# Kernel tuning notes

Measured on AMD Instinct MI355X. Metric: run time of the kernel, lower is better.

Reference implementation:

```python
import jax, jax.numpy as jnp
import numpy as np
import math

B, N, D = 128, 64, 2
H, M, L = 64, 64, 2
OMEGA = 1.0


def setup_inputs() -> dict:
    key = jax.random.key(0)
    ks = jax.random.split(key, 32)
    s = 0.1  # param scale
    rn = lambda k, shp: jax.random.normal(k, shp, dtype=jnp.float32) * s
    inp = {
        "x": jax.random.normal(ks[0], (B, N, D), dtype=jnp.float32),
        "spin": jnp.zeros((B, N, 1), jnp.float32),
        "node_w1": rn(ks[1], (D + 1, H)), "node_b1": rn(ks[2], (H,)),
        "node_w2": rn(ks[3], (H, H)), "node_b2": rn(ks[4], (H,)),
        "edge_w1": rn(ks[5], (D + 2, M)), "edge_b1": rn(ks[6], (M,)),
        "edge_w2": rn(ks[7], (M, M)), "edge_b2": rn(ks[8], (M,)),
        "v2e_w1": rn(ks[9], (L, H + M, M)), "v2e_b1": rn(ks[10], (L, M)),
        "v2e_w2": rn(ks[11], (L, M, M)), "v2e_b2": rn(ks[12], (L, M)),
        "e2v_w1": rn(ks[13], (L, M, H)), "e2v_b1": rn(ks[14], (L, H)),
        "e2v_w2": rn(ks[15], (L, H, H)), "e2v_b2": rn(ks[16], (L, H)),
        "head_w1": rn(ks[17], (H, H)), "head_b1": rn(ks[18], (H,)),
        "head_w2": rn(ks[19], (H, D)), "head_b2": rn(ks[20], (D,)),
        # bf_scale_init=0.3 -> softplus-inverse
        "scale": jnp.array([math.log(math.exp(0.3) - 1.0)], jnp.float32),
    }
    return inp


def _mlp(x, w1, b1, w2, b2, act):
    return act(x @ w1 + b1) @ w2 + b2


def reference(x, spin, node_w1, node_b1, node_w2, node_b2,
              edge_w1, edge_b1, edge_w2, edge_b2,
              v2e_w1, v2e_b1, v2e_w2, v2e_b2,
              e2v_w1, e2v_b1, e2v_w2, e2v_b2,
              head_w1, head_b1, head_w2, head_b2, scale):
    gelu = lambda t: jax.nn.gelu(t, approximate=False)  # torch exact GELU
    b, n, d = x.shape
    xs = x * jnp.float32(math.sqrt(OMEGA))
    # node embedding: [B,N,H]
    hv = _mlp(jnp.concatenate([xs, spin], -1), node_w1, node_b1, node_w2, node_b2, gelu)
    # dense pairwise edge features; dr[b,i,j] = xs[b,j] - xs[b,i]
    dr = xs[:, None, :, :] - xs[:, :, None, :]            # [B,N,N,D]
    r2 = jnp.sum(dr * dr, axis=-1, keepdims=True)          # [B,N,N,1]
    rr = jnp.sqrt(r2 + 1e-12)
    he = _mlp(jnp.concatenate([dr, rr, r2], -1), edge_w1, edge_b1, edge_w2, edge_b2, gelu)  # [B,N,N,M]
    # mask excludes self-edges (i==j) from aggregation (they were never created
    # in the original edge list; their dense entries never influence off-diag values)
    mask = (1.0 - jnp.eye(n, dtype=x.dtype))[None, :, :, None]
    inv = jnp.float32(1.0 / max(n - 1, 1))
    for l in range(v2e_w1.shape[0]):
        hvb = jnp.broadcast_to(hv[:, :, None, :], (b, n, n, hv.shape[-1]))  # source node i
        he = _mlp(jnp.concatenate([hvb, he], -1), v2e_w1[l], v2e_b1[l], v2e_w2[l], v2e_b2[l], gelu)
        m = _mlp(he, e2v_w1[l], e2v_b1[l], e2v_w2[l], e2v_b2[l], gelu)      # [B,N,N,H]
        hv = hv + jnp.sum(m * mask, axis=1) * inv           # scatter-add over sources i into j
    dx = _mlp(hv, head_w1, head_b1, head_w2, head_b2, jnp.tanh) * jax.nn.softplus(scale[0])
    return dx - jnp.mean(dx, axis=1, keepdims=True)
```

## Files before the change

kernel.cpp:

```cpp
#include <hip/hip_runtime.h>
#include <math.h>


typedef unsigned short u16;
typedef unsigned int u32;
typedef _Float16 half8 __attribute__((ext_vector_type(8)));
typedef __attribute__((ext_vector_type(4))) float floatx4;

#define TS 72

__device__ __forceinline__ float2 gelu2(float2 x) {
    const float K = 0.70710678118654752f;
    float ux = x.x * K,        uy = x.y * K;
    float sx = fabsf(ux),      sy = fabsf(uy);
    float tx = __builtin_amdgcn_rcpf(fmaf(0.3275911f, sx, 1.0f));
    float ty = __builtin_amdgcn_rcpf(fmaf(0.3275911f, sy, 1.0f));
    float Px = tx * fmaf(tx, fmaf(tx, fmaf(tx, fmaf(tx, 1.061405429f, -1.453152027f),
                                           1.421413741f), -0.284496736f), 0.254829592f);
    float Py = ty * fmaf(ty, fmaf(ty, fmaf(ty, fmaf(ty, 1.061405429f, -1.453152027f),
                                           1.421413741f), -0.284496736f), 0.254829592f);
    float ex = __expf(-sx * sx);
    float ey = __expf(-sy * sy);
    float rx = copysignf(fmaf(-Px, ex, 1.0f), ux);
    float ry = copysignf(fmaf(-Py, ey, 1.0f), uy);
    return make_float2(0.5f * x.x * (1.0f + rx), 0.5f * x.y * (1.0f + ry));
}
__device__ __forceinline__ float gelu_f(float x) {
    float u = x * 0.70710678118654752f;
    float s = fabsf(u);
    float t = __builtin_amdgcn_rcpf(fmaf(0.3275911f, s, 1.0f));
    float P = t * fmaf(t, fmaf(t, fmaf(t, fmaf(t, 1.061405429f, -1.453152027f),
                                        1.421413741f), -0.284496736f), 0.254829592f);
    float r = copysignf(fmaf(-P, __expf(-s * s), 1.0f), u);
    return 0.5f * x * (1.0f + r);
}

__global__ __launch_bounds__(256) void k_pre(
    const float* w0, const float* w1, const float* w2, const float* w3,
    const float* w4, const float* w5, const float* w6,
    const float* u2_0, const float* u2_1, const float* w1n, const float* hw1,
    _Float16* __restrict__ WF,
    float* __restrict__ u2_0T, float* __restrict__ u2_1T,
    float* __restrict__ w1nT, float* __restrict__ hw1T,
    const float* __restrict__ x, const float* __restrict__ spin,
    const float* __restrict__ nw1, const float* __restrict__ nb1,
    const float* __restrict__ nw2, const float* __restrict__ nb2,
    const float* __restrict__ w1_0, const float* __restrict__ b1_0,
    float* __restrict__ hv, float* __restrict__ p0)
{
    int blk = blockIdx.x;
    if (blk < 112) {
        int idx = blk * 256 + threadIdx.x;
        int s = idx >> 12, r = idx & 4095, k = r >> 6, n = r & 63;
        const float* W = s==0?w0: s==1?w1: s==2?w2: s==3?w3: s==4?w4: s==5?w5: w6;
        int kc = k >> 5, q = (k >> 3) & 3, jj = k & 7;
        WF[(((s * 2 + kc) * 64 + n) * 4 + q) * 8 + jj] = (_Float16)W[k * 64 + n];
    } else if (blk < 176) {
        int idx = (blk - 112) * 256 + threadIdx.x;
        int s = idx >> 12, r = idx & 4095, m = r >> 6, tc = r & 63;
        const float* W = s==0?u2_0: s==1?u2_1: s==2?w1n: hw1;
        float* WT      = s==0?u2_0T: s==1?u2_1T: s==2?w1nT: hw1T;
        WT[tc * 64 + m] = W[m * 64 + tc];
    } else {
        __shared__ float a[4][64];
        __shared__ float shv[4][64];
        int w = threadIdx.x >> 6, h = threadIdx.x & 63;
        int node = (blk - 176) * 4 + w;
        float2 xv = ((const float2*)x)[node];
        float sp = spin[node];
        float z = fmaf(xv.x, nw1[h], fmaf(xv.y, nw1[64 + h], fmaf(sp, nw1[128 + h], nb1[h])));
        a[w][h] = gelu_f(z);
        float acc = nb2[h];
        for (int k = 0; k < 64; ++k) acc = fmaf(a[w][k], nw2[k * 64 + h], acc);
        hv[node * 64 + h] = acc;
        shv[w][h] = acc;
        float pa = b1_0[h];
        for (int k = 0; k < 64; ++k) pa = fmaf(shv[w][k], w1_0[k * 64 + h], pa);
        p0[node * 64 + h] = pa;
    }
}

__device__ __forceinline__ void mfma_acc(
    const _Float16* __restrict__ tA, const _Float16* __restrict__ WF,
    int stage, int c, int quad, int nn, floatx4 acc[4])
{
    int sA = ((nn >> 2) & 3) << 3;
    #pragma unroll
    for (int kc = 0; kc < 2; ++kc) {
        half8 bf = *(const half8*)(WF + (((stage * 2 + kc) * 64 + c) * 4 + quad) * 8);
        int k0 = (kc * 32 + quad * 8) ^ sA;
        #pragma unroll
        for (int mt = 0; mt < 4; ++mt) {
            half8 af = *(const half8*)(tA + (mt * 16 + nn) * TS + k0);
            acc[mt] = __builtin_amdgcn_mfma_f32_16x16x32_f16(af, bf, acc[mt], 0, 0, 0);
        }
    }
}

__device__ __forceinline__ void init_bias(floatx4 acc[4], float bc) {
    #pragma unroll
    for (int mt = 0; mt < 4; ++mt) acc[mt] = (floatx4){bc, bc, bc, bc};
}
__device__ __forceinline__ void init_p(floatx4 acc[4], const float* __restrict__ p,
                                       int rowbase, int c, int quad) {
    #pragma unroll
    for (int mt = 0; mt < 4; ++mt)
        #pragma unroll
        for (int r = 0; r < 4; ++r)
            acc[mt][r] = p[(rowbase + mt * 16 + quad * 4 + r) * 64 + c];
}

__global__ __launch_bounds__(256, 8) void k_L0(
    const float* __restrict__ x,
    const float* __restrict__ ew1, const float* __restrict__ eb1,
    const float* __restrict__ eb2,
    const float* __restrict__ p0, const float* __restrict__ b2_0,
    const float* __restrict__ c1_0,
    const float* __restrict__ u2_0T, const float* __restrict__ c2_0,
    const _Float16* __restrict__ WF,
    const float* __restrict__ hv0, float* __restrict__ hv1,
    const float* __restrict__ w1nT, const float* __restrict__ b1n,
    float* __restrict__ p1,
    u16* __restrict__ he0g)
{
    __shared__ __align__(16) _Float16 tA[64 * TS];
    __shared__ float sgeo[256];
    __shared__ float sS[64];
    __shared__ float shv[64];
    int t = threadIdx.x, w = t >> 6, L = t & 63;
    int nn = L & 15, quad = L >> 4;
    int c = w * 16 + nn;
    int cw = c ^ (quad << 3);
    int b = blockIdx.x >> 6, j = blockIdx.x & 63;

    if (t < 64) {
        float2 xi = ((const float2*)x)[b * 64 + t];
        float2 xj = ((const float2*)x)[b * 64 + j];
        float d0 = xj.x - xi.x, d1 = xj.y - xi.y;
        float r2 = fmaf(d0, d0, d1 * d1);
        sgeo[t] = d0; sgeo[64 + t] = d1; sgeo[128 + t] = sqrtf(r2 + 1e-12f); sgeo[192 + t] = r2;
    }
    __syncthreads();
    {
        int m = t & 63, i0 = t >> 6;
        float wa = ew1[m], wb = ew1[64 + m], wc = ew1[128 + m], wd = ew1[192 + m], bm = eb1[m];
        #pragma unroll
        for (int k = 0; k < 16; k += 2) {
            int ia = i0 + k * 4, ib = i0 + (k + 1) * 4;
            float za = fmaf(sgeo[ia], wa, fmaf(sgeo[64 + ia], wb,
                       fmaf(sgeo[128 + ia], wc, fmaf(sgeo[192 + ia], wd, bm))));
            float zb = fmaf(sgeo[ib], wa, fmaf(sgeo[64 + ib], wb,
                       fmaf(sgeo[128 + ib], wc, fmaf(sgeo[192 + ib], wd, bm))));
            float2 g = gelu2(make_float2(za, zb));
            tA[ia * TS + (m ^ (((ia >> 2) & 3) << 3))] = (_Float16)g.x;
            tA[ib * TS + (m ^ (((ib >> 2) & 3) << 3))] = (_Float16)g.y;
        }
    }
    __syncthreads();

    floatx4 acc[4];
    init_bias(acc, eb2[c]);
    mfma_acc(tA, WF, 0, c, quad, nn, acc);
    __syncthreads();
    #pragma unroll
    for (int mt = 0; mt < 4; ++mt)
        #pragma unroll
        for (int r = 0; r < 4; ++r)
            tA[(mt * 16 + quad * 4 + r) * TS + cw] = (_Float16)acc[mt][r];
    __syncthreads();
    init_p(acc, p0, b * 64, c, quad);
    mfma_acc(tA, WF, 1, c, quad, nn, acc);
    __syncthreads();
    #pragma unroll
    for (int mt = 0; mt < 4; ++mt)
        #pragma unroll
        for (int rp = 0; rp < 4; rp += 2) {
            float2 g = gelu2(make_float2(acc[mt][rp], acc[mt][rp + 1]));
            tA[(mt * 16 + quad * 4 + rp) * TS + cw]     = (_Float16)g.x;
            tA[(mt * 16 + quad * 4 + rp + 1) * TS + cw] = (_Float16)g.y;
        }
    __syncthreads();
    init_bias(acc, b2_0[c]);
    mfma_acc(tA, WF, 2, c, quad, nn, acc);
    __syncthreads();
    {
        u16* dst = he0g + (size_t)blockIdx.x * 4096;
        #pragma unroll
        for (int mt = 0; mt < 4; ++mt)
            #pragma unroll
            for (int r = 0; r < 4; ++r) {
                int i = mt * 16 + quad * 4 + r;
                _Float16 hvv = (_Float16)acc[mt][r];
                tA[i * TS + cw] = hvv;
                dst[i * 64 + cw] = __builtin_bit_cast(u16, hvv);
            }
    }
    __syncthreads();
    init_bias(acc, c1_0[c]);
    mfma_acc(tA, WF, 3, c, quad, nn, acc);
    {
        float s = 0.f;
        #pragma unroll
        for (int mt = 0; mt < 4; ++mt)
            #pragma unroll
            for (int rp = 0; rp < 4; rp += 2) {
                int i = mt * 16 + quad * 4 + rp;
                float2 g = gelu2(make_float2(acc[mt][rp], acc[mt][rp + 1]));
                s += (i == j ? 0.f : g.x) + (i + 1 == j ? 0.f : g.y);
            }
        s += __shfl_xor(s, 16);
        s += __shfl_xor(s, 32);
        if (quad == 0) sS[c] = s;
    }
    __syncthreads();
    if (t < 64) {
        const float4* sv4 = (const float4*)sS;
        const float4* uv4 = (const float4*)(u2_0T + t * 64);
        float g = 0.f;
        #pragma unroll
        for (int m4 = 0; m4 < 16; ++m4) {
            float4 sv = sv4[m4], uv = uv4[m4];
            g = fmaf(sv.x, uv.x, fmaf(sv.y, uv.y, fmaf(sv.z, uv.z, fmaf(sv.w, uv.w, g))));
        }
        int o = blockIdx.x * 64 + t;
        float hvv = hv0[o] + g * (1.0f / 63.0f) + c2_0[t];
        hv1[o] = hvv;
        shv[t] = hvv;
        const float4* hv4 = (const float4*)shv;
        const float4* wv4 = (const float4*)(w1nT + t * 64);
        float pa = b1n[t];
        #pragma unroll
        for (int m4 = 0; m4 < 16; ++m4) {
            float4 sv = hv4[m4], uv = wv4[m4];
            pa = fmaf(sv.x, uv.x, fmaf(sv.y, uv.y, fmaf(sv.z, uv.z, fmaf(sv.w, uv.w, pa))));
        }
        p1[o] = pa;
    }
}

__global__ __launch_bounds__(256, 8) void k_L1(
    const u16* __restrict__ he0g,
    const float* __restrict__ p1, const float* __restrict__ b2_1,
    const float* __restrict__ c1_1,
    const float* __restrict__ u2_1T, const float* __restrict__ c2_1,
    const _Float16* __restrict__ WF,
    const float* __restrict__ hv1,
    const float* __restrict__ hw1T, const float* __restrict__ hb1,
    const float* __restrict__ hw2, const float* __restrict__ hb2,
    const float* __restrict__ scale, float* __restrict__ dx)
{
    __shared__ __align__(16) _Float16 tA[64 * TS];
    __shared__ float sS[64];
    __shared__ float shv[64];
    int t = threadIdx.x, w = t >> 6, L = t & 63;
    int nn = L & 15, quad = L >> 4;
    int c = w * 16 + nn;
    int cw = c ^ (quad << 3);
    int b = blockIdx.x >> 6, j = blockIdx.x & 63;

    {
        const u32* src = (const u32*)(he0g + (size_t)blockIdx.x * 4096);
        for (int qq = t; qq < 2048; qq += 256) {
            u32 v = src[qq];
            int i = qq >> 5, m2 = (qq & 31) * 2;
            *(u32*)((u16*)tA + i * TS + m2) = v;
        }
    }
    __syncthreads();

    floatx4 acc[4];
    init_p(acc, p1, b * 64, c, quad);
    mfma_acc(tA, WF, 4, c, quad, nn, acc);
    __syncthreads();
    #pragma unroll
    for (int mt = 0; mt < 4; ++mt)
        #pragma unroll
        for (int rp = 0; rp < 4; rp += 2) {
            float2 g = gelu2(make_float2(acc[mt][rp], acc[mt][rp + 1]));
            tA[(mt * 16 + quad * 4 + rp) * TS + cw]     = (_Float16)g.x;
            tA[(mt * 16 + quad * 4 + rp + 1) * TS + cw] = (_Float16)g.y;
        }
    __syncthreads();
    init_bias(acc, b2_1[c]);
    mfma_acc(tA, WF, 5, c, quad, nn, acc);
    __syncthreads();
    #pragma unroll
    for (int mt = 0; mt < 4; ++mt)
        #pragma unroll
        for (int r = 0; r < 4; ++r)
            tA[(mt * 16 + quad * 4 + r) * TS + cw] = (_Float16)acc[mt][r];
    __syncthreads();
    init_bias(acc, c1_1[c]);
    mfma_acc(tA, WF, 6, c, quad, nn, acc);
    {
        float s = 0.f;
        #pragma unroll
        for (int mt = 0; mt < 4; ++mt)
            #pragma unroll
            for (int rp = 0; rp < 4; rp += 2) {
                int i = mt * 16 + quad * 4 + rp;
                float2 g = gelu2(make_float2(acc[mt][rp], acc[mt][rp + 1]));
                s += (i == j ? 0.f : g.x) + (i + 1 == j ? 0.f : g.y);
            }
        s += __shfl_xor(s, 16);
        s += __shfl_xor(s, 32);
        if (quad == 0) sS[c] = s;
    }
    __syncthreads();
    if (t < 64) {
        const float4* sv4 = (const float4*)sS;
        const float4* uv4 = (const float4*)(u2_1T + t * 64);
        float g = 0.f;
        #pragma unroll
        for (int m4 = 0; m4 < 16; ++m4) {
            float4 sv = sv4[m4], uv = uv4[m4];
            g = fmaf(sv.x, uv.x, fmaf(sv.y, uv.y, fmaf(sv.z, uv.z, fmaf(sv.w, uv.w, g))));
        }
        float hv2 = hv1[blockIdx.x * 64 + t] + g * (1.0f / 63.0f) + c2_1[t];
        shv[t] = hv2;
        const float4* hv4 = (const float4*)shv;
        const float4* wv4 = (const float4*)(hw1T + t * 64);
        float a = hb1[t];
        #pragma unroll
        for (int m4 = 0; m4 < 16; ++m4) {
            float4 sv = hv4[m4], uv = wv4[m4];
            a = fmaf(sv.x, uv.x, fmaf(sv.y, uv.y, fmaf(sv.z, uv.z, fmaf(sv.w, uv.w, a))));
        }
        float t1 = tanhf(a);
        float d0 = t1 * hw2[t * 2], d1 = t1 * hw2[t * 2 + 1];
        #pragma unroll
        for (int off = 1; off <= 32; off <<= 1) { d0 += __shfl_xor(d0, off); d1 += __shfl_xor(d1, off); }
        if (t == 0) {
            float sp = log1pf(__expf(scale[0]));
            dx[blockIdx.x * 2 + 0] = (d0 + hb2[0]) * sp;
            dx[blockIdx.x * 2 + 1] = (d1 + hb2[1]) * sp;
        }
    }
}

__global__ __launch_bounds__(64) void k_mean(
    const float* __restrict__ dx, float* __restrict__ out)
{
    __shared__ float s0[64], s1[64];
    int b = blockIdx.x, j = threadIdx.x;
    float2 d = ((const float2*)dx)[b * 64 + j];
    s0[j] = d.x; s1[j] = d.y;
    __syncthreads();
    float m0 = 0.f, m1 = 0.f;
    for (int q = 0; q < 64; ++q) { m0 += s0[q]; m1 += s1[q]; }
    ((float2*)out)[b * 64 + j] = make_float2(d.x - m0 * (1.0f / 64.0f), d.y - m1 * (1.0f / 64.0f));
}

__global__ void k_beacon(float* out, float code) { out[0] = code; }

extern "C" void kernel_launch(void* const* d_in, const int* in_sizes, int n_in,
                              void* d_out, int out_size, void* d_ws, size_t ws_size,
                              hipStream_t stream)
{
    static const int exp_sizes[23] = {
        16384, 8192, 192, 64, 4096, 64,
        256, 64, 4096, 64,
        16384, 128, 8192, 128,
        8192, 128, 8192, 128,
        4096, 64, 128, 2, 1
    };
    float* hv0 = (float*)d_ws;
    float* hv1 = hv0 + 524288;
    float* p0  = hv1 + 524288;
    float* p1  = p0  + 524288;
    float* dx  = p1  + 524288;
    float* u2_0T = dx + 16384;
    float* u2_1T = u2_0T + 4096;
    float* w1nT  = u2_1T + 4096;
    float* hw1T  = w1nT + 4096;
    _Float16* WF = (_Float16*)(hw1T + 4096);
    u16* he0g  = (u16*)(WF + 28672);
    const size_t need = (size_t)((char*)(he0g + 33554432) - (char*)d_ws);

    int bad = -1;
    if (n_in != 23 || out_size != 16384) bad = 98;
    else if (ws_size < need) bad = 97;
    else for (int i = 0; i < 23; ++i)
        if (in_sizes[i] != exp_sizes[i]) { bad = i; break; }
    if (bad >= 0) {
        k_beacon<<<1, 1, 0, stream>>>((float*)d_out, 2e6f + bad * 1e4f);
        return;
    }

    const float* x      = (const float*)d_in[0];
    const float* spin   = (const float*)d_in[1];
    const float* nw1    = (const float*)d_in[2];
    const float* nb1    = (const float*)d_in[3];
    const float* nw2    = (const float*)d_in[4];
    const float* nb2    = (const float*)d_in[5];
    const float* ew1    = (const float*)d_in[6];
    const float* eb1    = (const float*)d_in[7];
    const float* ew2    = (const float*)d_in[8];
    const float* eb2    = (const float*)d_in[9];
    const float* v2e_w1 = (const float*)d_in[10];
    const float* v2e_b1 = (const float*)d_in[11];
    const float* v2e_w2 = (const float*)d_in[12];
    const float* v2e_b2 = (const float*)d_in[13];
    const float* e2v_w1 = (const float*)d_in[14];
    const float* e2v_b1 = (const float*)d_in[15];
    const float* e2v_w2 = (const float*)d_in[16];
    const float* e2v_b2 = (const float*)d_in[17];
    const float* hw1    = (const float*)d_in[18];
    const float* hb1    = (const float*)d_in[19];
    const float* hw2    = (const float*)d_in[20];
    const float* hb2    = (const float*)d_in[21];
    const float* scale  = (const float*)d_in[22];

    k_pre<<<2224, 256, 0, stream>>>(
        ew2, v2e_w1 + 4096, v2e_w2, e2v_w1, v2e_w1 + 12288, v2e_w2 + 4096, e2v_w1 + 4096,
        e2v_w2, e2v_w2 + 4096, v2e_w1 + 8192, hw1,
        WF, u2_0T, u2_1T, w1nT, hw1T,
        x, spin, nw1, nb1, nw2, nb2, v2e_w1, v2e_b1, hv0, p0);
    k_L0<<<8192, 256, 0, stream>>>(x, ew1, eb1, eb2,
        p0, v2e_b2, e2v_b1, u2_0T, e2v_b2,
        WF, hv0, hv1,
        w1nT, v2e_b1 + 64, p1,
        he0g);
    k_L1<<<8192, 256, 0, stream>>>(he0g,
        p1, v2e_b2 + 64, e2v_b1 + 64, u2_1T, e2v_b2 + 64,
        WF, hv1, hw1T, hb1, hw2, hb2, scale, dx);
    k_mean<<<128, 64, 0, stream>>>(dx, (float*)d_out);
}
```

Baseline: 256.0 us.

## Fold consecutive linear layers into precomputed fused weights and biases

Back-to-back linear maps with no activation between them (edge w2 into v2e w1, v2e w2 into e2v w1) are multiplied together in a prep kernel. The per-edge kernels then run 2 MFMA GEMM stages per layer instead of 3–4, and drop the matching LDS round-trips and barriers. The prep is split into two kernels because the node embedding now needs a folded bias. Folding weights changes fp16 rounding of the intermediates, and the exact gelu2 pair helper is replaced by a scalar gelu.

```diff
diff --git a/kernel.cpp b/kernel.cpp
--- a/kernel.cpp
+++ b/kernel.cpp
@@ -9,22 +9,6 @@
 
 #define TS 72
 
-__device__ __forceinline__ float2 gelu2(float2 x) {
-    const float K = 0.70710678118654752f;
-    float ux = x.x * K,        uy = x.y * K;
-    float sx = fabsf(ux),      sy = fabsf(uy);
-    float tx = __builtin_amdgcn_rcpf(fmaf(0.3275911f, sx, 1.0f));
-    float ty = __builtin_amdgcn_rcpf(fmaf(0.3275911f, sy, 1.0f));
-    float Px = tx * fmaf(tx, fmaf(tx, fmaf(tx, fmaf(tx, 1.061405429f, -1.453152027f),
-                                           1.421413741f), -0.284496736f), 0.254829592f);
-    float Py = ty * fmaf(ty, fmaf(ty, fmaf(ty, fmaf(ty, 1.061405429f, -1.453152027f),
-                                           1.421413741f), -0.284496736f), 0.254829592f);
-    float ex = __expf(-sx * sx);
-    float ey = __expf(-sy * sy);
-    float rx = copysignf(fmaf(-Px, ex, 1.0f), ux);
-    float ry = copysignf(fmaf(-Py, ey, 1.0f), uy);
-    return make_float2(0.5f * x.x * (1.0f + rx), 0.5f * x.y * (1.0f + ry));
-}
 __device__ __forceinline__ float gelu_f(float x) {
     float u = x * 0.70710678118654752f;
     float s = fabsf(u);
@@ -35,49 +19,78 @@
     return 0.5f * x * (1.0f + r);
 }
 
-__global__ __launch_bounds__(256) void k_pre(
-    const float* w0, const float* w1, const float* w2, const float* w3,
-    const float* w4, const float* w5, const float* w6,
-    const float* u2_0, const float* u2_1, const float* w1n, const float* hw1,
+__global__ __launch_bounds__(256) void k_pre1(
+    const float* __restrict__ ew2, const float* __restrict__ w1he0,
+    const float* __restrict__ w2_0, const float* __restrict__ u1_0,
+    const float* __restrict__ w1he1, const float* __restrict__ w2_1,
+    const float* __restrict__ u1_1,
+    const float* __restrict__ eb2, const float* __restrict__ b2_0,
+    const float* __restrict__ c1_0, const float* __restrict__ b2_1,
+    const float* __restrict__ c1_1,
+    const float* __restrict__ u2_0, const float* __restrict__ u2_1,
+    const float* __restrict__ w1n, const float* __restrict__ hw1,
     _Float16* __restrict__ WF,
+    float* __restrict__ biasA, float* __restrict__ biasB,
+    float* __restrict__ biasC, float* __restrict__ biasD,
     float* __restrict__ u2_0T, float* __restrict__ u2_1T,
-    float* __restrict__ w1nT, float* __restrict__ hw1T,
+    float* __restrict__ w1nT, float* __restrict__ hw1T)
+{
+    int blk = blockIdx.x;
+    if (blk < 64) {
+        int s = blk >> 4;
+        int idx = (blk & 15) * 256 + threadIdx.x;
+        int k = idx >> 6, n = idx & 63;
+        const float *A, *Bm;
+        if (s == 0)      { A = ew2;  Bm = w1he0; }
+        else if (s == 1) { A = w2_0; Bm = u1_0;  }
+        else if (s == 2) { A = w2_0; Bm = w1he1; }
+        else             { A = w2_1; Bm = u1_1;  }
+        float acc = 0.f;
+        for (int q = 0; q < 64; ++q) acc = fmaf(A[k * 64 + q], Bm[q * 64 + n], acc);
+        int kc = k >> 5, qd = (k >> 3) & 3, jj = k & 7;
+        WF[(((s * 2 + kc) * 64 + n) * 4 + qd) * 8 + jj] = (_Float16)acc;
+    } else if (blk == 64) {
+        int s = threadIdx.x >> 6, cc = threadIdx.x & 63;
+        const float *bv, *Bm, *add; float* dst;
+        if (s == 0)      { bv = eb2;  Bm = w1he0; add = nullptr; dst = biasA; }
+        else if (s == 1) { bv = b2_0; Bm = u1_0;  add = c1_0;    dst = biasB; }
+        else if (s == 2) { bv = b2_0; Bm = w1he1; add = nullptr; dst = biasC; }
+        else             { bv = b2_1; Bm = u1_1;  add = c1_1;    dst = biasD; }
+        float acc = add ? add[cc] : 0.f;
+        for (int q = 0; q < 64; ++q) acc = fmaf(bv[q], Bm[q * 64 + cc], acc);
+        dst[cc] = acc;
+    } else {
+        int idx = (blk - 65) * 256 + threadIdx.x;
+        int s = idx >> 12, r = idx & 4095, m = r >> 6, tc = r & 63;
+        const float* W = s == 0 ? u2_0 : s == 1 ? u2_1 : s == 2 ? w1n : hw1;
+        float* WT      = s == 0 ? u2_0T : s == 1 ? u2_1T : s == 2 ? w1nT : hw1T;
+        WT[tc * 64 + m] = W[m * 64 + tc];
+    }
+}
+
+__global__ __launch_bounds__(256) void k_pre2(
     const float* __restrict__ x, const float* __restrict__ spin,
     const float* __restrict__ nw1, const float* __restrict__ nb1,
     const float* __restrict__ nw2, const float* __restrict__ nb2,
     const float* __restrict__ w1_0, const float* __restrict__ b1_0,
+    const float* __restrict__ biasA,
     float* __restrict__ hv, float* __restrict__ p0)
 {
-    int blk = blockIdx.x;
-    if (blk < 112) {
-        int idx = blk * 256 + threadIdx.x;
-        int s = idx >> 12, r = idx & 4095, k = r >> 6, n = r & 63;
-        const float* W = s==0?w0: s==1?w1: s==2?w2: s==3?w3: s==4?w4: s==5?w5: w6;
-        int kc = k >> 5, q = (k >> 3) & 3, jj = k & 7;
-        WF[(((s * 2 + kc) * 64 + n) * 4 + q) * 8 + jj] = (_Float16)W[k * 64 + n];
-    } else if (blk < 176) {
-        int idx = (blk - 112) * 256 + threadIdx.x;
-        int s = idx >> 12, r = idx & 4095, m = r >> 6, tc = r & 63;
-        const float* W = s==0?u2_0: s==1?u2_1: s==2?w1n: hw1;
-        float* WT      = s==0?u2_0T: s==1?u2_1T: s==2?w1nT: hw1T;
-        WT[tc * 64 + m] = W[m * 64 + tc];
-    } else {
-        __shared__ float a[4][64];
-        __shared__ float shv[4][64];
-        int w = threadIdx.x >> 6, h = threadIdx.x & 63;
-        int node = (blk - 176) * 4 + w;
-        float2 xv = ((const float2*)x)[node];
-        float sp = spin[node];
-        float z = fmaf(xv.x, nw1[h], fmaf(xv.y, nw1[64 + h], fmaf(sp, nw1[128 + h], nb1[h])));
-        a[w][h] = gelu_f(z);
-        float acc = nb2[h];
-        for (int k = 0; k < 64; ++k) acc = fmaf(a[w][k], nw2[k * 64 + h], acc);
-        hv[node * 64 + h] = acc;
-        shv[w][h] = acc;
-        float pa = b1_0[h];
-        for (int k = 0; k < 64; ++k) pa = fmaf(shv[w][k], w1_0[k * 64 + h], pa);
-        p0[node * 64 + h] = pa;
-    }
+    __shared__ float a[4][64];
+    __shared__ float shv[4][64];
+    int w = threadIdx.x >> 6, h = threadIdx.x & 63;
+    int node = blockIdx.x * 4 + w;
+    float2 xv = ((const float2*)x)[node];
+    float sp = spin[node];
+    float z = fmaf(xv.x, nw1[h], fmaf(xv.y, nw1[64 + h], fmaf(sp, nw1[128 + h], nb1[h])));
+    a[w][h] = gelu_f(z);
+    float acc = nb2[h];
+    for (int k = 0; k < 64; ++k) acc = fmaf(a[w][k], nw2[k * 64 + h], acc);
+    hv[node * 64 + h] = acc;
+    shv[w][h] = acc;
+    float pa = b1_0[h] + biasA[h];
+    for (int k = 0; k < 64; ++k) pa = fmaf(shv[w][k], w1_0[k * 64 + h], pa);
+    p0[node * 64 + h] = pa;
 }
 
 __device__ __forceinline__ void mfma_acc(
@@ -113,13 +126,13 @@
 __global__ __launch_bounds__(256, 8) void k_L0(
     const float* __restrict__ x,
     const float* __restrict__ ew1, const float* __restrict__ eb1,
-    const float* __restrict__ eb2,
-    const float* __restrict__ p0, const float* __restrict__ b2_0,
-    const float* __restrict__ c1_0,
+    const float* __restrict__ p0,
+    const float* __restrict__ biasB,
     const float* __restrict__ u2_0T, const float* __restrict__ c2_0,
     const _Float16* __restrict__ WF,
     const float* __restrict__ hv0, float* __restrict__ hv1,
     const float* __restrict__ w1nT, const float* __restrict__ b1n,
+    const float* __restrict__ biasC,
     float* __restrict__ p1,
     u16* __restrict__ he0g)
 {
@@ -145,43 +158,18 @@
         int m = t & 63, i0 = t >> 6;
         float wa = ew1[m], wb = ew1[64 + m], wc = ew1[128 + m], wd = ew1[192 + m], bm = eb1[m];
         #pragma unroll
-        for (int k = 0; k < 16; k += 2) {
-            int ia = i0 + k * 4, ib = i0 + (k + 1) * 4;
-            float za = fmaf(sgeo[ia], wa, fmaf(sgeo[64 + ia], wb,
-                       fmaf(sgeo[128 + ia], wc, fmaf(sgeo[192 + ia], wd, bm))));
-            float zb = fmaf(sgeo[ib], wa, fmaf(sgeo[64 + ib], wb,
-                       fmaf(sgeo[128 + ib], wc, fmaf(sgeo[192 + ib], wd, bm))));
-            float2 g = gelu2(make_float2(za, zb));
-            tA[ia * TS + (m ^ (((ia >> 2) & 3) << 3))] = (_Float16)g.x;
-            tA[ib * TS + (m ^ (((ib >> 2) & 3) << 3))] = (_Float16)g.y;
+        for (int k = 0; k < 16; ++k) {
+            int i = i0 + k * 4;
+            float z = fmaf(sgeo[i], wa, fmaf(sgeo[64 + i], wb,
+                      fmaf(sgeo[128 + i], wc, fmaf(sgeo[192 + i], wd, bm))));
+            tA[i * TS + (m ^ (((i >> 2) & 3) << 3))] = (_Float16)gelu_f(z);
         }
     }
     __syncthreads();
 
     floatx4 acc[4];
-    init_bias(acc, eb2[c]);
+    init_p(acc, p0, b * 64, c, quad);
     mfma_acc(tA, WF, 0, c, quad, nn, acc);
-    __syncthreads();
-    #pragma unroll
-    for (int mt = 0; mt < 4; ++mt)
-        #pragma unroll
-        for (int r = 0; r < 4; ++r)
-            tA[(mt * 16 + quad * 4 + r) * TS + cw] = (_Float16)acc[mt][r];
-    __syncthreads();
-    init_p(acc, p0, b * 64, c, quad);
-    mfma_acc(tA, WF, 1, c, quad, nn, acc);
-    __syncthreads();
-    #pragma unroll
-    for (int mt = 0; mt < 4; ++mt)
-        #pragma unroll
-        for (int rp = 0; rp < 4; rp += 2) {
-            float2 g = gelu2(make_float2(acc[mt][rp], acc[mt][rp + 1]));
-            tA[(mt * 16 + quad * 4 + rp) * TS + cw]     = (_Float16)g.x;
-            tA[(mt * 16 + quad * 4 + rp + 1) * TS + cw] = (_Float16)g.y;
-        }
-    __syncthreads();
-    init_bias(acc, b2_0[c]);
-    mfma_acc(tA, WF, 2, c, quad, nn, acc);
     __syncthreads();
     {
         u16* dst = he0g + (size_t)blockIdx.x * 4096;
@@ -190,23 +178,23 @@
             #pragma unroll
             for (int r = 0; r < 4; ++r) {
                 int i = mt * 16 + quad * 4 + r;
-                _Float16 hvv = (_Float16)acc[mt][r];
-                tA[i * TS + cw] = hvv;
-                dst[i * 64 + cw] = __builtin_bit_cast(u16, hvv);
+                _Float16 y = (_Float16)gelu_f(acc[mt][r]);
+                tA[i * TS + cw] = y;
+                dst[i * 64 + cw] = __builtin_bit_cast(u16, y);
             }
     }
     __syncthreads();
-    init_bias(acc, c1_0[c]);
-    mfma_acc(tA, WF, 3, c, quad, nn, acc);
+    init_bias(acc, biasB[c]);
+    mfma_acc(tA, WF, 1, c, quad, nn, acc);
     {
         float s = 0.f;
         #pragma unroll
         for (int mt = 0; mt < 4; ++mt)
             #pragma unroll
-            for (int rp = 0; rp < 4; rp += 2) {
-                int i = mt * 16 + quad * 4 + rp;
-                float2 g = gelu2(make_float2(acc[mt][rp], acc[mt][rp + 1]));
-                s += (i == j ? 0.f : g.x) + (i + 1 == j ? 0.f : g.y);
+            for (int r = 0; r < 4; ++r) {
+                int i = mt * 16 + quad * 4 + r;
+                float g = gelu_f(acc[mt][r]);
+                s += (i == j) ? 0.f : g;
             }
         s += __shfl_xor(s, 16);
         s += __shfl_xor(s, 32);
@@ -228,7 +216,7 @@
         shv[t] = hvv;
         const float4* hv4 = (const float4*)shv;
         const float4* wv4 = (const float4*)(w1nT + t * 64);
-        float pa = b1n[t];
+        float pa = b1n[t] + biasC[t];
         #pragma unroll
         for (int m4 = 0; m4 < 16; ++m4) {
             float4 sv = hv4[m4], uv = wv4[m4];
@@ -240,8 +228,8 @@
 
 __global__ __launch_bounds__(256, 8) void k_L1(
     const u16* __restrict__ he0g,
-    const float* __restrict__ p1, const float* __restrict__ b2_1,
-    const float* __restrict__ c1_1,
+    const float* __restrict__ p1,
+    const float* __restrict__ biasD,
     const float* __restrict__ u2_1T, const float* __restrict__ c2_1,
     const _Float16* __restrict__ WF,
     const float* __restrict__ hv1,
@@ -270,37 +258,25 @@
 
     floatx4 acc[4];
     init_p(acc, p1, b * 64, c, quad);
-    mfma_acc(tA, WF, 4, c, quad, nn, acc);
+    mfma_acc(tA, WF, 2, c, quad, nn, acc);
     __syncthreads();
     #pragma unroll
     for (int mt = 0; mt < 4; ++mt)
         #pragma unroll
-        for (int rp = 0; rp < 4; rp += 2) {
-            float2 g = gelu2(make_float2(acc[mt][rp], acc[mt][rp + 1]));
-            tA[(mt * 16 + quad * 4 + rp) * TS + cw]     = (_Float16)g.x;
-            tA[(mt * 16 + quad * 4 + rp + 1) * TS + cw] = (_Float16)g.y;
-        }
-    __syncthreads();
-    init_bias(acc, b2_1[c]);
-    mfma_acc(tA, WF, 5, c, quad, nn, acc);
-    __syncthreads();
-    #pragma unroll
-    for (int mt = 0; mt < 4; ++mt)
-        #pragma unroll
         for (int r = 0; r < 4; ++r)
-            tA[(mt * 16 + quad * 4 + r) * TS + cw] = (_Float16)acc[mt][r];
-    __syncthreads();
-    init_bias(acc, c1_1[c]);
-    mfma_acc(tA, WF, 6, c, quad, nn, acc);
+            tA[(mt * 16 + quad * 4 + r) * TS + cw] = (_Float16)gelu_f(acc[mt][r]);
+    __syncthreads();
+    init_bias(acc, biasD[c]);
+    mfma_acc(tA, WF, 3, c, quad, nn, acc);
     {
         float s = 0.f;
         #pragma unroll
         for (int mt = 0; mt < 4; ++mt)
             #pragma unroll
-            for (int rp = 0; rp < 4; rp += 2) {
-                int i = mt * 16 + quad * 4 + rp;
-                float2 g = gelu2(make_float2(acc[mt][rp], acc[mt][rp + 1]));
-                s += (i == j ? 0.f : g.x) + (i + 1 == j ? 0.f : g.y);
+            for (int r = 0; r < 4; ++r) {
+                int i = mt * 16 + quad * 4 + r;
+                float g = gelu_f(acc[mt][r]);
+                s += (i == j) ? 0.f : g;
             }
         s += __shfl_xor(s, 16);
         s += __shfl_xor(s, 32);
@@ -373,8 +349,12 @@
     float* u2_1T = u2_0T + 4096;
     float* w1nT  = u2_1T + 4096;
     float* hw1T  = w1nT + 4096;
-    _Float16* WF = (_Float16*)(hw1T + 4096);
-    u16* he0g  = (u16*)(WF + 28672);
+    float* biasA = hw1T + 4096;
+    float* biasB = biasA + 64;
+    float* biasC = biasB + 64;
+    float* biasD = biasC + 64;
+    _Float16* WF = (_Float16*)(biasD + 64);
+    u16* he0g  = (u16*)(WF + 16384);
     const size_t need = (size_t)((char*)(he0g + 33554432) - (char*)d_ws);
 
     int bad = -1;
@@ -411,18 +391,22 @@
     const float* hb2    = (const float*)d_in[21];
     const float* scale  = (const float*)d_in[22];
 
-    k_pre<<<2224, 256, 0, stream>>>(
-        ew2, v2e_w1 + 4096, v2e_w2, e2v_w1, v2e_w1 + 12288, v2e_w2 + 4096, e2v_w1 + 4096,
+    k_pre1<<<129, 256, 0, stream>>>(
+        ew2, v2e_w1 + 4096, v2e_w2, e2v_w1,
+        v2e_w1 + 12288, v2e_w2 + 4096, e2v_w1 + 4096,
+        eb2, v2e_b2, e2v_b1, v2e_b2 + 64, e2v_b1 + 64,
         e2v_w2, e2v_w2 + 4096, v2e_w1 + 8192, hw1,
-        WF, u2_0T, u2_1T, w1nT, hw1T,
-        x, spin, nw1, nb1, nw2, nb2, v2e_w1, v2e_b1, hv0, p0);
-    k_L0<<<8192, 256, 0, stream>>>(x, ew1, eb1, eb2,
-        p0, v2e_b2, e2v_b1, u2_0T, e2v_b2,
+        WF, biasA, biasB, biasC, biasD,
+        u2_0T, u2_1T, w1nT, hw1T);
+    k_pre2<<<2048, 256, 0, stream>>>(x, spin, nw1, nb1, nw2, nb2,
+                                     v2e_w1, v2e_b1, biasA, hv0, p0);
+    k_L0<<<8192, 256, 0, stream>>>(x, ew1, eb1,
+        p0, biasB, u2_0T, e2v_b2,
         WF, hv0, hv1,
-        w1nT, v2e_b1 + 64, p1,
+        w1nT, v2e_b1 + 64, biasC, p1,
         he0g);
     k_L1<<<8192, 256, 0, stream>>>(he0g,
-        p1, v2e_b2 + 64, e2v_b1 + 64, u2_1T, e2v_b2 + 64,
+        p1, biasD, u2_1T, e2v_b2 + 64,
         WF, hv1, hw1T, hb1, hw2, hb2, scale, dx);
     k_mean<<<128, 64, 0, stream>>>(dx, (float*)d_out);
 }
```

Result: faster. 243.6 us (-4.8%).
